# Kernel optimization log

Hardware: AMD Instinct MI355X
Metric: run time of the kernel (lower is better)

Reference implementation:

```python
import jax, jax.numpy as jnp
import numpy as np

B, T, C, H = 4, 1024, 512, 4
D = C // H
N_LAYER, LAYER_ID = 12, 1


def setup_inputs() -> dict:
    key = jax.random.key(0)
    ks = jax.random.split(key, 10)
    w = lambda k, shape: 0.02 * jax.random.normal(k, shape, dtype=jnp.float32)

    r01 = LAYER_ID / (N_LAYER - 1)          # ratio_0_to_1
    r1a0 = 1.0 - LAYER_ID / N_LAYER          # ratio_1_to_almost0
    i = np.arange(C, dtype=np.float32)
    time_decay = (-5.0 + 8.0 * (i / (C - 1)) ** (0.7 + 1.3 * r01)).astype(np.float32)
    xv = i / C
    tm_q = (xv ** r1a0).astype(np.float32)[None, None, :]
    tm_k = (xv ** r1a0).astype(np.float32)[None, None, :]
    tm_v = ((xv ** r1a0) + 0.3 * r01).astype(np.float32)[None, None, :]
    tm_g = (xv ** (0.5 * r1a0)).astype(np.float32)[None, None, :]

    return dict(
        x=jax.random.normal(ks[0], (B, T, C), dtype=jnp.float32),
        ln1_g=jnp.ones((C,), jnp.float32), ln1_b=jnp.zeros((C,), jnp.float32),
        ln2_g=jnp.ones((C,), jnp.float32), ln2_b=jnp.zeros((C,), jnp.float32),
        time_decay=jnp.asarray(time_decay),
        tm_q=jnp.asarray(tm_q), tm_k=jnp.asarray(tm_k),
        tm_v=jnp.asarray(tm_v), tm_g=jnp.asarray(tm_g),
        Wq=w(ks[1], (C, C)), Wk=w(ks[2], (C, C)), Wv=w(ks[3], (C, C)),
        Wg=w(ks[4], (C, C)), Wo=w(ks[5], (C, C)),
        rms_scale=jnp.ones((C,), jnp.float32),
        W1=w(ks[6], (4 * C, C)), W2=w(ks[7], (C, 4 * C)),
    )


def layernorm(x, g, b, eps=1e-5):
    m = x.mean(-1, keepdims=True)
    v = ((x - m) ** 2).mean(-1, keepdims=True)
    return g * (x - m) / jnp.sqrt(v + eps) + b


def rmsnorm(x, scale, eps=1e-8):
    # matches: norm = ||x||_2 / sqrt(dim); out = scale * x / (norm + eps)
    norm = jnp.sqrt(jnp.sum(x * x, axis=-1, keepdims=True)) / (x.shape[-1] ** 0.5)
    return scale * (x / (norm + eps))


def lnssm_scan(q, k, v, lam):
    """Decayed linear-attention scan. q,k,v: [B,T,H,D]; lam: [H,D] (decay over k index).
    Returns S: [B,T,H,D] = q_t^T A_t, Zs: [B,T,H] = q_t . z_t."""
    qT, kT, vT = (jnp.moveaxis(a, 1, 0) for a in (q, k, v))  # [T,B,H,D]
    Bq = q.shape[0]
    A0 = jnp.zeros((Bq, q.shape[2], q.shape[3], q.shape[3]), q.dtype)
    z0 = jnp.zeros((Bq, q.shape[2], q.shape[3]), q.dtype)

    def step(carry, inp):
        A, z = carry
        qt, kt, vt = inp
        A = lam[None, :, :, None] * A + kt[..., None] * vt[..., None, :]  # [B,H,Dk,Dv]
        z = lam[None] * z + kt                                            # [B,H,Dk]
        St = jnp.einsum('bhi,bhij->bhj', qt, A)
        Zt = jnp.einsum('bhi,bhi->bh', qt, z)
        return (A, z), (St, Zt)

    _, (S, Zs) = jax.lax.scan(step, (A0, z0), (qT, kT, vT))
    return jnp.moveaxis(S, 0, 1), jnp.moveaxis(Zs, 0, 1)


def reference(x, ln1_g, ln1_b, ln2_g, ln2_b, time_decay, tm_q, tm_k, tm_v, tm_g,
              Wq, Wk, Wv, Wg, Wo, rms_scale, W1, W2):
    Bx, Tx, Cx = x.shape
    Hh, Dd = H, Cx // H

    # --- TimeMix on ln1(x) ---
    h = layernorm(x, ln1_g, ln1_b)
    xx = jnp.concatenate([jnp.zeros_like(h[:, :1]), h[:, :-1]], axis=1)  # time shift
    xq = h * tm_q + xx * (1 - tm_q)
    xk = h * tm_k + xx * (1 - tm_k)
    xv_ = h * tm_v + xx * (1 - tm_v)
    xg = h * tm_g + xx * (1 - tm_g)
    q = xq @ Wq.T
    k = xk @ Wk.T
    v = xv_ @ Wv.T
    g = jax.nn.sigmoid(xg @ Wg.T)
    q = jnp.exp(rmsnorm(q, rms_scale))
    k = jnp.exp(rmsnorm(k, rms_scale))

    lam = jnp.exp(-jnp.exp(time_decay)).reshape(Hh, Dd)
    qh = q.reshape(Bx, Tx, Hh, Dd)
    kh = k.reshape(Bx, Tx, Hh, Dd)
    vh = v.reshape(Bx, Tx, Hh, Dd)
    S, Zs = lnssm_scan(qh, kh, vh, lam)
    att = (S / Zs[..., None]).reshape(Bx, Tx, Cx)
    att = (g * att) @ Wo.T
    x = x + att

    # --- ChannelMix on ln2(x) ---
    h2 = layernorm(x, ln2_g, ln2_b)
    x = x + jax.nn.gelu(h2 @ W1.T, approximate=False) @ W2.T
    return x
```

## Files before the change

### kernel.cpp

```cpp
#include <hip/hip_runtime.h>
#include <math.h>

#define Bb 4
#define Tt 1024
#define Cc 512
#define Hh 4
#define Dd 128
#define Mrows (Bb*Tt)
#define NC 32
#define CL 32
#define AUGSZ (Dd*(Dd+1))
#define AUGSTRIDE (16*AUGSZ)

typedef unsigned short u16;
typedef __attribute__((ext_vector_type(8))) short bf16x8;
typedef __attribute__((ext_vector_type(4))) float f32x4;

__device__ __forceinline__ float readlane_f(float v, int lane) {
  return __uint_as_float(__builtin_amdgcn_readlane(__float_as_uint(v), lane));
}
__device__ __forceinline__ u16 f2bf(float f) {
  unsigned u = __float_as_uint(f);
  unsigned r = (u + 0x7fffu + ((u >> 16) & 1u)) >> 16;
  return (u16)r;
}
__device__ __forceinline__ unsigned pack2(float a, float b) {
  return (unsigned)f2bf(a) | ((unsigned)f2bf(b) << 16);
}

__global__ __launch_bounds__(256) void ln_kernel(const float* __restrict__ x,
    const float* __restrict__ g, const float* __restrict__ bta, float* __restrict__ out)
{
  int row = blockIdx.x, tid = threadIdx.x;
  const float* xr = x + (size_t)row * Cc;
  float v0 = xr[tid], v1 = xr[tid + 256];
  float s = v0 + v1, s2 = v0*v0 + v1*v1;
  #pragma unroll
  for (int off = 32; off > 0; off >>= 1) {
    s  += __shfl_down(s,  off, 64);
    s2 += __shfl_down(s2, off, 64);
  }
  __shared__ float rs[4], rq[4];
  int w = tid >> 6;
  if ((tid & 63) == 0) { rs[w] = s; rq[w] = s2; }
  __syncthreads();
  float S  = rs[0]+rs[1]+rs[2]+rs[3];
  float S2 = rq[0]+rq[1]+rq[2]+rq[3];
  float mean = S * (1.0f/Cc);
  float var  = S2 * (1.0f/Cc) - mean*mean;
  float inv = rsqrtf(var + 1e-5f);
  out[(size_t)row*Cc + tid]       = g[tid]     * (v0-mean)*inv + bta[tid];
  out[(size_t)row*Cc + tid + 256] = g[tid+256] * (v1-mean)*inv + bta[tid+256];
}

__global__ __launch_bounds__(256) void ln2b_kernel(const float* __restrict__ x,
    const float* __restrict__ p0, const float* __restrict__ p1,
    const float* __restrict__ g, const float* __restrict__ bta,
    float* __restrict__ x1, u16* __restrict__ out)
{
  int row = blockIdx.x, tid = threadIdx.x;
  size_t r0 = (size_t)row * Cc + tid, r1 = r0 + 256;
  float v0 = x[r0] + p0[r0] + p1[r0];
  float v1 = x[r1] + p0[r1] + p1[r1];
  x1[r0] = v0; x1[r1] = v1;
  float s = v0 + v1, s2 = v0*v0 + v1*v1;
  #pragma unroll
  for (int off = 32; off > 0; off >>= 1) {
    s  += __shfl_down(s,  off, 64);
    s2 += __shfl_down(s2, off, 64);
  }
  __shared__ float rs[4], rq[4];
  int w = tid >> 6;
  if ((tid & 63) == 0) { rs[w] = s; rq[w] = s2; }
  __syncthreads();
  float S  = rs[0]+rs[1]+rs[2]+rs[3];
  float S2 = rq[0]+rq[1]+rq[2]+rq[3];
  float mean = S * (1.0f/Cc);
  float var  = S2 * (1.0f/Cc) - mean*mean;
  float inv = rsqrtf(var + 1e-5f);
  int c0 = tid, c1 = tid + 256;
  float o0 = g[c0] * (v0-mean)*inv + bta[c0];
  float o1 = g[c1] * (v1-mean)*inv + bta[c1];
  out[((size_t)(c0 >> 3) * Mrows + row) * 8 + (c0 & 7)] = f2bf(o0);
  out[((size_t)(c1 >> 3) * Mrows + row) * 8 + (c1 & 7)] = f2bf(o1);
}

__device__ __forceinline__ void mix_one(const float* tm, int c0,
    float4 ha, float4 hb, float4 xa, float4 xb, u16* dst, size_t i8)
{
  float4 ta = *(const float4*)(tm + c0);
  float4 tb = *(const float4*)(tm + c0 + 4);
  uint4 o;
  o.x = pack2(ha.x*ta.x + xa.x*(1.f-ta.x), ha.y*ta.y + xa.y*(1.f-ta.y));
  o.y = pack2(ha.z*ta.z + xa.z*(1.f-ta.z), ha.w*ta.w + xa.w*(1.f-ta.w));
  o.z = pack2(hb.x*tb.x + xb.x*(1.f-tb.x), hb.y*tb.y + xb.y*(1.f-tb.y));
  o.w = pack2(hb.z*tb.z + xb.z*(1.f-tb.z), hb.w*tb.w + xb.w*(1.f-tb.w));
  *(uint4*)(dst + i8) = o;
}

__global__ __launch_bounds__(256) void mix_kernel(const float* __restrict__ h,
    const float* __restrict__ tmq, const float* __restrict__ tmk,
    const float* __restrict__ tmv, const float* __restrict__ tmg,
    u16* __restrict__ xqb, u16* __restrict__ xkb,
    u16* __restrict__ xvb, u16* __restrict__ xgb)
{
  int i = blockIdx.x * 256 + threadIdx.x;
  int m = i & 4095, c0 = (i >> 12) << 3;
  const float* hp = h + (size_t)m*Cc + c0;
  float4 ha = *(const float4*)hp, hb = *(const float4*)(hp + 4);
  float4 xa = make_float4(0,0,0,0), xb = make_float4(0,0,0,0);
  if (m & 1023) { xa = *(const float4*)(hp - Cc); xb = *(const float4*)(hp - Cc + 4); }
  size_t i8 = (size_t)i * 8;
  mix_one(tmq, c0, ha, hb, xa, xb, xqb, i8);
  mix_one(tmk, c0, ha, hb, xa, xb, xkb, i8);
  mix_one(tmv, c0, ha, hb, xa, xb, xvb, i8);
  mix_one(tmg, c0, ha, hb, xa, xb, xgb, i8);
}

__global__ __launch_bounds__(256) void wconv_kernel(const float* __restrict__ src,
    u16* __restrict__ out, int K, int nshift)
{
  int i = blockIdx.x * 256 + threadIdx.x;
  int n = i & ((1 << nshift) - 1), kg = i >> nshift;
  const float* p = src + (size_t)n * K + kg * 8;
  float4 a = *(const float4*)p, b = *(const float4*)(p + 4);
  uint4 o;
  o.x = pack2(a.x, a.y); o.y = pack2(a.z, a.w);
  o.z = pack2(b.x, b.y); o.w = pack2(b.z, b.w);
  *(uint4*)(out + (size_t)i * 8) = o;
}

__global__ __launch_bounds__(256) void wconv5_kernel(const float* __restrict__ s0,
    const float* __restrict__ s1, const float* __restrict__ s2,
    const float* __restrict__ s3, const float* __restrict__ s4,
    u16* __restrict__ out)
{
  int wsel = blockIdx.x >> 7;
  const float* src = wsel == 0 ? s0 : wsel == 1 ? s1 : wsel == 2 ? s2 : wsel == 3 ? s3 : s4;
  int i = (blockIdx.x & 127) * 256 + threadIdx.x;
  int n = i & 511, kg = i >> 9;
  const float* p = src + (size_t)n * 512 + kg * 8;
  float4 a = *(const float4*)p, b = *(const float4*)(p + 4);
  uint4 o;
  o.x = pack2(a.x, a.y); o.y = pack2(a.z, a.w);
  o.z = pack2(b.x, b.y); o.w = pack2(b.z, b.w);
  *(uint4*)(out + (size_t)wsel * 262144 + (size_t)i * 8) = o;
}

template<int MR, int NR, int KR>
__device__ __forceinline__ void gemm_core(const u16* __restrict__ A,
    const u16* __restrict__ W, const float* __restrict__ res,
    float* __restrict__ outf, u16* __restrict__ outb, int act,
    int m0, int n0, u16* Asm, u16* Bsm)
{
  const int tid = threadIdx.x, w = tid >> 6, l = tid & 63;
  const int wr = w >> 1, wc = w & 1;
  f32x4 acc[4][4];
  #pragma unroll
  for (int i = 0; i < 4; ++i)
    #pragma unroll
    for (int j = 0; j < 4; ++j) acc[i][j] = (f32x4){0.f,0.f,0.f,0.f};
  const int kgl = l >> 4, rl = l & 15;
  const int q = w * 4;

  #define STAGE(KT, BUF) do {                                               \
    _Pragma("unroll")                                                       \
    for (int ii = 0; ii < 4; ++ii) {                                        \
      int qq = q + ii;                                                      \
      int isB = qq >> 3, idx = qq & 7, kg = idx >> 1, hf = idx & 1;         \
      const u16* src = isB                                                  \
        ? W + ((size_t)((KT)*4 + kg) * NR + n0 + hf*64 + l) * 8             \
        : A + ((size_t)((KT)*4 + kg) * MR + m0 + hf*64 + l) * 8;            \
      u16* dst = (isB ? Bsm : Asm) + (BUF)*4096 + (kg * 128 + hf * 64) * 8; \
      __builtin_amdgcn_global_load_lds(                                     \
          (const __attribute__((address_space(1))) void*)src,               \
          (__attribute__((address_space(3))) void*)dst, 16, 0, 0);          \
    }                                                                       \
  } while (0)

  constexpr int nk = KR >> 5;
  STAGE(0, 0); STAGE(1, 1); STAGE(2, 2);
  for (int kt = 0; kt < nk; ++kt) {
    const int cur = kt & 3;
    if (kt < nk - 2)       asm volatile("s_waitcnt vmcnt(8)" ::: "memory");
    else if (kt == nk - 2) asm volatile("s_waitcnt vmcnt(4)" ::: "memory");
    else                   asm volatile("s_waitcnt vmcnt(0)" ::: "memory");
    __builtin_amdgcn_s_barrier();
    bf16x8 af[4], bfr[4];
    #pragma unroll
    for (int f = 0; f < 4; ++f)
      af[f] = *(const bf16x8*)&Asm[cur*4096 + (kgl*128 + wr*64 + f*16 + rl) * 8];
    #pragma unroll
    for (int f = 0; f < 4; ++f)
      bfr[f] = *(const bf16x8*)&Bsm[cur*4096 + (kgl*128 + wc*64 + f*16 + rl) * 8];
    if (kt + 3 < nk) STAGE(kt + 3, (kt + 3) & 3);
    __builtin_amdgcn_s_setprio(1);
    #pragma unroll
    for (int i = 0; i < 4; ++i)
      #pragma unroll
      for (int j = 0; j < 4; ++j)
        acc[i][j] = __builtin_amdgcn_mfma_f32_16x16x32_bf16(af[i], bfr[j], acc[i][j], 0, 0, 0);
    __builtin_amdgcn_s_setprio(0);
  }
  #undef STAGE

  const int rbase = (l >> 4) * 4, cn = l & 15;
  #pragma unroll
  for (int i = 0; i < 4; ++i) {
    #pragma unroll
    for (int j = 0; j < 4; ++j) {
      #pragma unroll
      for (int r = 0; r < 4; ++r) {
        int m = m0 + wr*64 + i*16 + rbase + r;
        int n = n0 + wc*64 + j*16 + cn;
        float vv = acc[i][j][r];
        if (res) vv += res[(size_t)m * NR + n];
        if (act == 1) vv = 0.5f*vv*(1.f + erff(vv * 0.70710678118f));
        else if (act == 2) vv = 1.f/(1.f + expf(-vv));
        if (outb) outb[((size_t)(n >> 3) * MR + m) * 8 + (n & 7)] = f2bf(vv);
        else outf[(size_t)m * NR + n] = vv;
      }
    }
  }
}

__global__ __launch_bounds__(256) void gemm_qkvg(const u16* __restrict__ xall,
    const u16* __restrict__ Wall, float* __restrict__ outall)
{
  __shared__ __align__(16) u16 Asm[4*4096];
  __shared__ __align__(16) u16 Bsm[4*4096];
  int z = blockIdx.z;
  const size_t E = (size_t)Mrows * Cc;
  gemm_core<Mrows,512,512>(xall + z*E, Wall + (size_t)z*262144, nullptr,
            outall + z*E, nullptr, z == 3 ? 2 : 0,
            blockIdx.y * 128, blockIdx.x * 128, Asm, Bsm);
}

__global__ __launch_bounds__(256) void gemm_wo(const u16* __restrict__ A,
    const u16* __restrict__ W, float* __restrict__ pbuf)
{
  __shared__ __align__(16) u16 Asm[4*4096];
  __shared__ __align__(16) u16 Bsm[4*4096];
  int z = blockIdx.z;
  const size_t E = (size_t)Mrows * Cc;
  gemm_core<Mrows,512,256>(A + (size_t)z*32*Mrows*8, W + (size_t)z*32*512*8, nullptr,
            pbuf + z*E, nullptr, 0, blockIdx.y * 128, blockIdx.x * 128, Asm, Bsm);
}

__global__ __launch_bounds__(256) void gemm_w1(const u16* __restrict__ A,
    const u16* __restrict__ W, u16* __restrict__ outb)
{
  __shared__ __align__(16) u16 Asm[4*4096];
  __shared__ __align__(16) u16 Bsm[4*4096];
  gemm_core<Mrows,2048,512>(A, W, nullptr, nullptr, outb, 1,
            blockIdx.y * 128, blockIdx.x * 128, Asm, Bsm);
}

__global__ __launch_bounds__(256) void gemm_w2(const u16* __restrict__ A,
    const u16* __restrict__ W, float* __restrict__ pbuf)
{
  __shared__ __align__(16) u16 Asm[4*4096];
  __shared__ __align__(16) u16 Bsm[4*4096];
  int z = blockIdx.z;
  const size_t E = (size_t)Mrows * Cc;
  gemm_core<Mrows,512,512>(A + (size_t)z*64*Mrows*8, W + (size_t)z*64*512*8, nullptr,
            pbuf + z*E, nullptr, 0, blockIdx.y * 128, blockIdx.x * 128, Asm, Bsm);
}

__global__ __launch_bounds__(256) void reduce4_kernel(const float* __restrict__ x1,
    const float* __restrict__ p, float* __restrict__ out)
{
  const size_t E = (size_t)Mrows * Cc;
  size_t f = ((size_t)blockIdx.x * 256 + threadIdx.x) * 4;
  float4 a = *(const float4*)(x1 + f);
  float4 q0 = *(const float4*)(p + f);
  float4 q1 = *(const float4*)(p + E + f);
  float4 q2 = *(const float4*)(p + 2*E + f);
  float4 q3 = *(const float4*)(p + 3*E + f);
  float4 o;
  o.x = a.x + q0.x + q1.x + q2.x + q3.x;
  o.y = a.y + q0.y + q1.y + q2.y + q3.y;
  o.z = a.z + q0.z + q1.z + q2.z + q3.z;
  o.w = a.w + q0.w + q1.w + q2.w + q3.w;
  *(float4*)(out + f) = o;
}

__global__ __launch_bounds__(256) void rmsexp_kernel(float* __restrict__ qm,
    float* __restrict__ km, const float* __restrict__ scale)
{
  int row = blockIdx.x, tid = threadIdx.x;
  float* xr = (blockIdx.y ? km : qm) + (size_t)row * Cc;
  float v0 = xr[tid], v1 = xr[tid+256];
  float s2 = v0*v0 + v1*v1;
  #pragma unroll
  for (int off = 32; off > 0; off >>= 1) s2 += __shfl_down(s2, off, 64);
  __shared__ float rq[4];
  int w = tid >> 6;
  if ((tid & 63) == 0) rq[w] = s2;
  __syncthreads();
  float S2 = rq[0]+rq[1]+rq[2]+rq[3];
  float norm = sqrtf(S2) * 0.044194173824159216f;
  float r = 1.f / (norm + 1e-8f);
  xr[tid]     = expf(scale[tid]     * v0 * r);
  xr[tid+256] = expf(scale[tid+256] * v1 * r);
}

__global__ __launch_bounds__(256) void chunk_state_kernel(const float* __restrict__ k,
    const float* __restrict__ v, const float* __restrict__ td, float* __restrict__ Aug)
{
  __shared__ float k_lds[CL][Dd];
  __shared__ float v_lds[CL][Dd];
  int blk = blockIdx.x; int c = blk & (NC-1); int bh = blk >> 5;
  int b = bh >> 2, h = bh & 3;
  int tid = threadIdx.x;
  size_t base = ((size_t)b*Tt + (size_t)c*CL)*Cc + h*Dd;
  #pragma unroll
  for (int r = 0; r < 4; ++r) {
    int idx4 = r*256 + tid;
    int s = idx4 >> 5; int i4 = (idx4 & 31) << 2;
    *(float4*)&k_lds[s][i4] = *(const float4*)&k[base + (size_t)s*Cc + i4];
    *(float4*)&v_lds[s][i4] = *(const float4*)&v[base + (size_t)s*Cc + i4];
  }
  __syncthreads();
  int iq = tid >> 3; int i0 = iq << 2;
  int jg = tid & 7;  int j0 = jg << 4;
  float lam4[4], powv[4], zacc[4];
  #pragma unroll
  for (int ci=0; ci<4; ++ci) {
    lam4[ci] = expf(-expf(td[h*Dd + i0 + ci]));
    powv[ci] = 1.f; zacc[ci] = 0.f;
  }
  float acc[4][16];
  #pragma unroll
  for (int ci=0; ci<4; ++ci)
    #pragma unroll
    for (int jj=0; jj<16; ++jj) acc[ci][jj] = 0.f;

  for (int s = CL-1; s >= 0; --s) {
    float4 k4 = *(const float4*)&k_lds[s][i0];
    float kw0 = powv[0]*k4.x, kw1 = powv[1]*k4.y, kw2 = powv[2]*k4.z, kw3 = powv[3]*k4.w;
    zacc[0]+=kw0; zacc[1]+=kw1; zacc[2]+=kw2; zacc[3]+=kw3;
    #pragma unroll
    for (int q4 = 0; q4 < 4; ++q4) {
      float4 v4 = *(const float4*)&v_lds[s][j0 + q4*4];
      float vv[4] = {v4.x, v4.y, v4.z, v4.w};
      #pragma unroll
      for (int u=0; u<4; ++u) {
        acc[0][q4*4+u] += kw0*vv[u];
        acc[1][q4*4+u] += kw1*vv[u];
        acc[2][q4*4+u] += kw2*vv[u];
        acc[3][q4*4+u] += kw3*vv[u];
      }
    }
    powv[0]*=lam4[0]; powv[1]*=lam4[1]; powv[2]*=lam4[2]; powv[3]*=lam4[3];
  }
  float* aug = Aug + ((size_t)c*16 + bh)*AUGSZ;
  #pragma unroll
  for (int jj=0; jj<16; ++jj) {
    int j = j0 + jj;
    float4 wv = make_float4(acc[0][jj], acc[1][jj], acc[2][jj], acc[3][jj]);
    *(float4*)&aug[(size_t)j*Dd + i0] = wv;
  }
  if (jg == 0)
    *(float4*)&aug[(size_t)Dd*Dd + i0] = make_float4(zacc[0],zacc[1],zacc[2],zacc[3]);
}

__global__ __launch_bounds__(256) void combine_kernel(float* __restrict__ Aug,
    const float* __restrict__ td)
{
  int idx = blockIdx.x*256 + threadIdx.x;
  if (idx >= AUGSZ) return;
  int bh = blockIdx.y; int h = bh & 3;
  int i = idx & (Dd-1);
  float lamL = expf(-expf(td[h*Dd + i]) * (float)CL);
  float* p = Aug + (size_t)bh*AUGSZ + idx;
  float prev = 0.f;
  for (int c = 0; c < NC; ++c) {
    float val = p[(size_t)c*AUGSTRIDE];
    p[(size_t)c*AUGSTRIDE] = prev;
    prev = lamL*prev + val;
  }
}

__global__ __launch_bounds__(256, 2) void scan_out_kernel(const float* __restrict__ q,
    const float* __restrict__ k, const float* __restrict__ v,
    const float* __restrict__ td, const float* __restrict__ Aug,
    const float* __restrict__ gmat, u16* __restrict__ out)
{
  __shared__ float part[4*16*128];
  __shared__ float zpart[4*16];
  int blk = blockIdx.x; int c = blk & (NC-1); int bh = blk >> 5;
  int b = bh >> 2, h = bh & 3;
  int tid = threadIdx.x; int w = tid >> 6, l = tid & 63;
  const size_t base = ((size_t)b*Tt)*Cc + h*Dd;
  const float* augc = Aug + ((size_t)c*16 + bh)*AUGSZ;
  int iq = w*32 + (l & 31);
  float lamv = expf(-expf(td[h*Dd + iq]));
  float lam_s[32];
  #pragma unroll
  for (int ii = 0; ii < 32; ++ii) lam_s[ii] = readlane_f(lamv, ii);

  float A0[32], A1[32];
  {
    const float4* p0 = (const float4*)(augc + (size_t)l*Dd + w*32);
    const float4* p1 = (const float4*)(augc + (size_t)(l+64)*Dd + w*32);
    #pragma unroll
    for (int r = 0; r < 8; ++r) {
      float4 a = p0[r];
      A0[4*r+0]=a.x; A0[4*r+1]=a.y; A0[4*r+2]=a.z; A0[4*r+3]=a.w;
      float4 bb = p1[r];
      A1[4*r+0]=bb.x; A1[4*r+1]=bb.y; A1[4*r+2]=bb.z; A1[4*r+3]=bb.w;
    }
  }
  float z = 0.f;
  if (l < 32) z = augc[(size_t)Dd*Dd + w*32 + l];

  int t0 = c*CL;
  const float* qk_ptr = (l < 32) ? q : k;
  size_t pbase = base + (size_t)t0*Cc;
  float qk = qk_ptr[pbase + iq];
  float v0 = v[pbase + l];
  float v1 = v[pbase + l + 64];

  #pragma unroll
  for (int half = 0; half < 2; ++half) {
    for (int tl = 0; tl < 16; ++tl) {
      int t = half*16 + tl;
      float qk_c = qk, v0c = v0, v1c = v1;
      if (t + 1 < CL) {
        size_t nb = pbase + (size_t)(t+1)*Cc;
        qk = qk_ptr[nb + iq];
        v0 = v[nb + l];
        v1 = v[nb + l + 64];
      }
      float s0 = 0.f, s1 = 0.f;
      #pragma unroll
      for (int ii = 0; ii < 32; ++ii) {
        float qs = readlane_f(qk_c, ii);
        float ks = readlane_f(qk_c, 32 + ii);
        A0[ii] = lam_s[ii]*A0[ii] + ks*v0c;
        A1[ii] = lam_s[ii]*A1[ii] + ks*v1c;
        s0 += qs * A0[ii];
        s1 += qs * A1[ii];
      }
      part[(w*16 + tl)*128 + l]      = s0;
      part[(w*16 + tl)*128 + l + 64] = s1;
      float kme = __shfl(qk_c, (l & 31) + 32);
      float p = 0.f;
      if (l < 32) { z = lamv*z + kme; p = qk_c * z; }
      #pragma unroll
      for (int off = 16; off > 0; off >>= 1) p += __shfl_down(p, off);
      if (l == 0) zpart[w*16 + tl] = p;
    }
    __syncthreads();
    #pragma unroll
    for (int r = 0; r < 8; ++r) {
      int lin = r*256 + tid; int tt = lin >> 7; int j = lin & 127;
      float sv = part[tt*128 + j] + part[(16+tt)*128 + j]
               + part[(32+tt)*128 + j] + part[(48+tt)*128 + j];
      float zv = zpart[tt] + zpart[16+tt] + zpart[32+tt] + zpart[48+tt];
      int m = b*Tt + t0 + half*16 + tt;
      int cc = h*Dd + j;
      float gv = gmat[(size_t)m*Cc + cc];
      out[((size_t)(cc >> 3) * Mrows + m) * 8 + (cc & 7)] = f2bf(gv * sv / zv);
    }
    __syncthreads();
  }
}

extern "C" void kernel_launch(void* const* d_in, const int* in_sizes, int n_in,
                              void* d_out, int out_size, void* d_ws, size_t ws_size,
                              hipStream_t stream) {
  const float* x    = (const float*)d_in[0];
  const float* ln1g = (const float*)d_in[1];
  const float* ln1b = (const float*)d_in[2];
  const float* ln2g = (const float*)d_in[3];
  const float* ln2b = (const float*)d_in[4];
  const float* td   = (const float*)d_in[5];
  const float* tmq  = (const float*)d_in[6];
  const float* tmk  = (const float*)d_in[7];
  const float* tmv  = (const float*)d_in[8];
  const float* tmg  = (const float*)d_in[9];
  const float* Wq   = (const float*)d_in[10];
  const float* Wk   = (const float*)d_in[11];
  const float* Wv   = (const float*)d_in[12];
  const float* Wg   = (const float*)d_in[13];
  const float* Wo   = (const float*)d_in[14];
  const float* rsc  = (const float*)d_in[15];
  const float* W1   = (const float*)d_in[16];
  const float* W2   = (const float*)d_in[17];
  float* ws = (float*)d_ws;
  const size_t E = (size_t)Mrows*Cc;
  float* s0 = ws;
  float* s1 = ws + E;
  float* s2 = ws + 2*E;
  float* s3 = ws + 3*E;
  float* x1 = ws + 4*E;
  u16* xqb = (u16*)(ws + 5*E);
  u16* xkb = xqb + E;
  u16* xvb = xkb + E;
  u16* xgb = xvb + E;
  float* Aug = ws + 7*E;
  u16* midb = (u16*)Aug;
  float* wreg = ws + 7*E + (size_t)NC*16*AUGSZ;
  u16* Wqb = (u16*)wreg;
  u16* W1b = Wqb + 5*262144;
  u16* W2b = W1b + 1048576;
  u16* Wob = Wqb + 4*262144;
  u16* gattb = xqb;
  u16* h2b   = xkb;

  wconv5_kernel<<<640,256,0,stream>>>(Wq, Wk, Wv, Wg, Wo, Wqb);
  wconv_kernel<<<512,256,0,stream>>>(W1, W1b, 512, 11);
  wconv_kernel<<<512,256,0,stream>>>(W2, W2b, 2048, 9);

  ln_kernel<<<Mrows,256,0,stream>>>(x, ln1g, ln1b, s0);
  mix_kernel<<<1024,256,0,stream>>>(s0, tmq,tmk,tmv,tmg, xqb,xkb,xvb,xgb);
  gemm_qkvg<<<dim3(4,32,4),256,0,stream>>>(xqb, Wqb, s0);
  rmsexp_kernel<<<dim3(Mrows,2),256,0,stream>>>(s0, s1, rsc);
  chunk_state_kernel<<<16*NC,256,0,stream>>>(s1, s2, td, Aug);
  combine_kernel<<<dim3((AUGSZ+255)/256,16),256,0,stream>>>(Aug, td);
  scan_out_kernel<<<16*NC,256,0,stream>>>(s0, s1, s2, td, Aug, s3, gattb);
  gemm_wo<<<dim3(4,32,2),256,0,stream>>>(gattb, Wob, s2);
  ln2b_kernel<<<Mrows,256,0,stream>>>(x, s2, s3, ln2g, ln2b, x1, h2b);
  gemm_w1<<<dim3(16,32),256,0,stream>>>(h2b, W1b, midb);
  gemm_w2<<<dim3(4,32,4),256,0,stream>>>(midb, W2b, s0);
  reduce4_kernel<<<2048,256,0,stream>>>(x1, s0, (float*)d_out);
}
```

Measured before the change: 191.5 us.

## Replace sequential per-chunk scan with MFMA chunked linear-attention output

Result: faster. 173.8 us (-9.3%).

```diff
diff --git a/kernel.cpp b/kernel.cpp
--- a/kernel.cpp
+++ b/kernel.cpp
@@ -11,6 +11,7 @@
 #define CL 32
 #define AUGSZ (Dd*(Dd+1))
 #define AUGSTRIDE (16*AUGSZ)
+#define AUGB_CB 18432
 
 typedef unsigned short u16;
 typedef __attribute__((ext_vector_type(8))) short bf16x8;
@@ -365,106 +366,195 @@
     *(float4*)&aug[(size_t)Dd*Dd + i0] = make_float4(zacc[0],zacc[1],zacc[2],zacc[3]);
 }
 
-__global__ __launch_bounds__(256) void combine_kernel(float* __restrict__ Aug,
-    const float* __restrict__ td)
+__global__ __launch_bounds__(256) void combine_kernel(const float* __restrict__ Aug,
+    const float* __restrict__ td, u16* __restrict__ Augb)
 {
   int idx = blockIdx.x*256 + threadIdx.x;
-  if (idx >= AUGSZ) return;
   int bh = blockIdx.y; int h = bh & 3;
-  int i = idx & (Dd-1);
+  int j = idx >> 7, i = idx & 127;
+  size_t aoff = (size_t)(i >> 3) * 1152 + (size_t)j * 8 + (i & 7);
+  if (j >= 129) {
+    for (int c = 0; c < NC; ++c)
+      Augb[((size_t)c*16 + bh)*AUGB_CB + aoff] = 0;
+    return;
+  }
   float lamL = expf(-expf(td[h*Dd + i]) * (float)CL);
-  float* p = Aug + (size_t)bh*AUGSZ + idx;
+  const float* p = Aug + (size_t)bh*AUGSZ + (size_t)j*Dd + i;
   float prev = 0.f;
   for (int c = 0; c < NC; ++c) {
     float val = p[(size_t)c*AUGSTRIDE];
-    p[(size_t)c*AUGSTRIDE] = prev;
+    Augb[((size_t)c*16 + bh)*AUGB_CB + aoff] = f2bf(prev);
     prev = lamL*prev + val;
   }
 }
 
-__global__ __launch_bounds__(256, 2) void scan_out_kernel(const float* __restrict__ q,
-    const float* __restrict__ k, const float* __restrict__ v,
-    const float* __restrict__ td, const float* __restrict__ Aug,
-    const float* __restrict__ gmat, u16* __restrict__ out)
-{
-  __shared__ float part[4*16*128];
-  __shared__ float zpart[4*16];
-  int blk = blockIdx.x; int c = blk & (NC-1); int bh = blk >> 5;
-  int b = bh >> 2, h = bh & 3;
-  int tid = threadIdx.x; int w = tid >> 6, l = tid & 63;
-  const size_t base = ((size_t)b*Tt)*Cc + h*Dd;
-  const float* augc = Aug + ((size_t)c*16 + bh)*AUGSZ;
-  int iq = w*32 + (l & 31);
-  float lamv = expf(-expf(td[h*Dd + iq]));
-  float lam_s[32];
-  #pragma unroll
-  for (int ii = 0; ii < 32; ++ii) lam_s[ii] = readlane_f(lamv, ii);
-
-  float A0[32], A1[32];
+__global__ __launch_bounds__(256, 2) void scan_mfma_kernel(
+    const float* __restrict__ q, const float* __restrict__ k,
+    const float* __restrict__ v, const float* __restrict__ td,
+    const u16* __restrict__ Augb, const float* __restrict__ gmat,
+    u16* __restrict__ out)
+{
+  __shared__ float k_lds[32*192];
+  __shared__ u16  qfrag[32*128];
+  __shared__ u16  vfrag[4*1152];
+  __shared__ float P32[32*33];
+  __shared__ u16  pfrag[32*32];
+  __shared__ float lam_lds[128];
+  __shared__ float zbuf[32];
+
+  const int tid = threadIdx.x;
+  const int blk = blockIdx.x; const int c = blk & 31, bh = blk >> 5;
+  const int b = bh >> 2, h = bh & 3;
+  const int w = tid >> 6, l = tid & 63;
+  const int t = (w << 3) + (l >> 3);
+  const int is = l & 7;
+
+  if (tid < 128) lam_lds[tid] = expf(-expf(td[h*Dd + tid]));
+
+  const size_t rowbase = ((size_t)(b*Tt + c*CL + t))*Cc + h*Dd + is*16;
+
+  float qv[16];
   {
-    const float4* p0 = (const float4*)(augc + (size_t)l*Dd + w*32);
-    const float4* p1 = (const float4*)(augc + (size_t)(l+64)*Dd + w*32);
-    #pragma unroll
-    for (int r = 0; r < 8; ++r) {
-      float4 a = p0[r];
-      A0[4*r+0]=a.x; A0[4*r+1]=a.y; A0[4*r+2]=a.z; A0[4*r+3]=a.w;
-      float4 bb = p1[r];
-      A1[4*r+0]=bb.x; A1[4*r+1]=bb.y; A1[4*r+2]=bb.z; A1[4*r+3]=bb.w;
-    }
-  }
-  float z = 0.f;
-  if (l < 32) z = augc[(size_t)Dd*Dd + w*32 + l];
-
-  int t0 = c*CL;
-  const float* qk_ptr = (l < 32) ? q : k;
-  size_t pbase = base + (size_t)t0*Cc;
-  float qk = qk_ptr[pbase + iq];
-  float v0 = v[pbase + l];
-  float v1 = v[pbase + l + 64];
-
-  #pragma unroll
-  for (int half = 0; half < 2; ++half) {
-    for (int tl = 0; tl < 16; ++tl) {
-      int t = half*16 + tl;
-      float qk_c = qk, v0c = v0, v1c = v1;
-      if (t + 1 < CL) {
-        size_t nb = pbase + (size_t)(t+1)*Cc;
-        qk = qk_ptr[nb + iq];
-        v0 = v[nb + l];
-        v1 = v[nb + l + 64];
+    #pragma unroll
+    for (int c4 = 0; c4 < 4; ++c4) {
+      float4 q4 = *(const float4*)(q + rowbase + c4*4);
+      qv[c4*4+0]=q4.x; qv[c4*4+1]=q4.y; qv[c4*4+2]=q4.z; qv[c4*4+3]=q4.w;
+    }
+    float lt = (float)(t + 1);
+    u16 qt[16];
+    #pragma unroll
+    for (int e = 0; e < 16; ++e) {
+      float el2 = -expf(td[h*Dd + is*16 + e]) * 1.4426950408889634f;
+      qt[e] = f2bf(qv[e] * exp2f(el2 * lt));
+    }
+    #pragma unroll
+    for (int hf = 0; hf < 2; ++hf) {
+      int k8 = is*2 + hf;
+      uint4 pk;
+      pk.x = (unsigned)qt[hf*8+0] | ((unsigned)qt[hf*8+1]<<16);
+      pk.y = (unsigned)qt[hf*8+2] | ((unsigned)qt[hf*8+3]<<16);
+      pk.z = (unsigned)qt[hf*8+4] | ((unsigned)qt[hf*8+5]<<16);
+      pk.w = (unsigned)qt[hf*8+6] | ((unsigned)qt[hf*8+7]<<16);
+      *(uint4*)&qfrag[t*128 + ((k8 ^ (t&7))<<3)] = pk;
+    }
+  }
+  #pragma unroll
+  for (int c4 = 0; c4 < 4; ++c4)
+    *(float4*)&k_lds[t*192 + is*24 + c4*4] = *(const float4*)(k + rowbase + c4*4);
+  #pragma unroll
+  for (int c4 = 0; c4 < 4; ++c4) {
+    float4 v4 = *(const float4*)(v + rowbase + c4*4);
+    int j0 = is*16 + c4*4;
+    vfrag[(t>>3)*1152 + (j0+0)*8 + (t&7)] = f2bf(v4.x);
+    vfrag[(t>>3)*1152 + (j0+1)*8 + (t&7)] = f2bf(v4.y);
+    vfrag[(t>>3)*1152 + (j0+2)*8 + (t&7)] = f2bf(v4.z);
+    vfrag[(t>>3)*1152 + (j0+3)*8 + (t&7)] = f2bf(v4.w);
+  }
+  if (tid < 32) vfrag[(tid>>3)*1152 + 128*8 + (tid&7)] = 0x3F80;
+  if (tid < 240) {
+    #pragma unroll
+    for (int u = 0; u < 2; ++u) {
+      int e = tid*2 + u;
+      int ig = e / 120, rem = e % 120;
+      vfrag[ig*1152 + (129 + rem/8)*8 + (rem&7)] = 0;
+    }
+  }
+  __syncthreads();
+
+  {
+    float lamr[16], wrun[16];
+    #pragma unroll
+    for (int e4 = 0; e4 < 4; ++e4) {
+      float4 l4 = *(const float4*)&lam_lds[is*16 + e4*4];
+      lamr[e4*4+0]=l4.x; lamr[e4*4+1]=l4.y; lamr[e4*4+2]=l4.z; lamr[e4*4+3]=l4.w;
+    }
+    #pragma unroll
+    for (int e = 0; e < 16; ++e) wrun[e] = 1.f;
+    const int smax = (w << 3) + 7;
+    for (int s = smax; s >= 0; --s) {
+      float dot = 0.f;
+      #pragma unroll
+      for (int c4 = 0; c4 < 4; ++c4) {
+        float4 k4 = *(const float4*)&k_lds[s*192 + is*24 + c4*4];
+        dot = fmaf(qv[c4*4+0], k4.x*wrun[c4*4+0], dot);
+        dot = fmaf(qv[c4*4+1], k4.y*wrun[c4*4+1], dot);
+        dot = fmaf(qv[c4*4+2], k4.z*wrun[c4*4+2], dot);
+        dot = fmaf(qv[c4*4+3], k4.w*wrun[c4*4+3], dot);
       }
-      float s0 = 0.f, s1 = 0.f;
+      dot += __shfl_xor(dot, 1);
+      dot += __shfl_xor(dot, 2);
+      dot += __shfl_xor(dot, 4);
+      bool act = (s <= t);
+      if (act && is == 0) P32[t*33 + s] = dot;
+      if (act) {
+        #pragma unroll
+        for (int e = 0; e < 16; ++e) wrun[e] *= lamr[e];
+      }
+    }
+  }
+  __syncthreads();
+  {
+    int tt = tid >> 3, s0 = (tid & 7) * 4;
+    #pragma unroll
+    for (int ss = 0; ss < 4; ++ss) {
+      int s = s0 + ss;
+      float val = (s <= tt) ? P32[tt*33 + s] : 0.f;
+      pfrag[tt*32 + (((s>>3) ^ (tt&3))<<3) + (s&7)] = f2bf(val);
+    }
+  }
+  __syncthreads();
+
+  const int tau = w >> 1;
+  const int jt0 = (w & 1) ? 5 : 0;
+  const int njt = (w & 1) ? 4 : 5;
+  const int rl = l & 15, kg = l >> 4;
+  const int trow = tau*16 + rl;
+  const u16* augb_base = Augb + ((size_t)c*16 + bh)*AUGB_CB;
+
+  bf16x8 aq[4];
+  #pragma unroll
+  for (int kk = 0; kk < 4; ++kk)
+    aq[kk] = *(const bf16x8*)&qfrag[trow*128 + ((((kk<<2)+kg) ^ (trow&7))<<3)];
+  bf16x8 ap = *(const bf16x8*)&pfrag[trow*32 + ((kg ^ (trow&3))<<3)];
+
+  f32x4 acc[5];
+  #pragma unroll
+  for (int u = 0; u < 5; ++u) acc[u] = (f32x4){0.f,0.f,0.f,0.f};
+
+  #pragma unroll
+  for (int u = 0; u < 5; ++u) {
+    if (u < njt) {
+      int jt = jt0 + u;
       #pragma unroll
-      for (int ii = 0; ii < 32; ++ii) {
-        float qs = readlane_f(qk_c, ii);
-        float ks = readlane_f(qk_c, 32 + ii);
-        A0[ii] = lam_s[ii]*A0[ii] + ks*v0c;
-        A1[ii] = lam_s[ii]*A1[ii] + ks*v1c;
-        s0 += qs * A0[ii];
-        s1 += qs * A1[ii];
+      for (int kk = 0; kk < 4; ++kk) {
+        bf16x8 bfr = *(const bf16x8*)&augb_base[(size_t)(((kk<<2)+kg)*1152 + (jt*16 + rl)*8)];
+        acc[u] = __builtin_amdgcn_mfma_f32_16x16x32_bf16(aq[kk], bfr, acc[u], 0, 0, 0);
       }
-      part[(w*16 + tl)*128 + l]      = s0;
-      part[(w*16 + tl)*128 + l + 64] = s1;
-      float kme = __shfl(qk_c, (l & 31) + 32);
-      float p = 0.f;
-      if (l < 32) { z = lamv*z + kme; p = qk_c * z; }
+      bf16x8 bv = *(const bf16x8*)&vfrag[kg*1152 + (jt*16 + rl)*8];
+      acc[u] = __builtin_amdgcn_mfma_f32_16x16x32_bf16(ap, bv, acc[u], 0, 0, 0);
+    }
+  }
+  if ((w & 1) && rl == 0) {
+    #pragma unroll
+    for (int r = 0; r < 4; ++r) zbuf[tau*16 + kg*4 + r] = acc[3][r];
+  }
+  __syncthreads();
+
+  const int nout = (w & 1) ? 3 : 5;
+  #pragma unroll
+  for (int u = 0; u < 5; ++u) {
+    if (u < nout) {
+      int jt = jt0 + u;
+      int cc = h*Dd + jt*16 + rl;
       #pragma unroll
-      for (int off = 16; off > 0; off >>= 1) p += __shfl_down(p, off);
-      if (l == 0) zpart[w*16 + tl] = p;
-    }
-    __syncthreads();
-    #pragma unroll
-    for (int r = 0; r < 8; ++r) {
-      int lin = r*256 + tid; int tt = lin >> 7; int j = lin & 127;
-      float sv = part[tt*128 + j] + part[(16+tt)*128 + j]
-               + part[(32+tt)*128 + j] + part[(48+tt)*128 + j];
-      float zv = zpart[tt] + zpart[16+tt] + zpart[32+tt] + zpart[48+tt];
-      int m = b*Tt + t0 + half*16 + tt;
-      int cc = h*Dd + j;
-      float gv = gmat[(size_t)m*Cc + cc];
-      out[((size_t)(cc >> 3) * Mrows + m) * 8 + (cc & 7)] = f2bf(gv * sv / zv);
-    }
-    __syncthreads();
+      for (int r = 0; r < 4; ++r) {
+        int tr = tau*16 + kg*4 + r;
+        int m = b*Tt + c*CL + tr;
+        float zv = zbuf[tr];
+        float gv = gmat[(size_t)m*Cc + cc];
+        out[((size_t)(cc >> 3) * Mrows + m) * 8 + (cc & 7)] = f2bf(gv * acc[u][r] / zv);
+      }
+    }
   }
 }
 
@@ -507,6 +597,7 @@
   u16* W1b = Wqb + 5*262144;
   u16* W2b = W1b + 1048576;
   u16* Wob = Wqb + 4*262144;
+  u16* Augb = W2b + 1048576;
   u16* gattb = xqb;
   u16* h2b   = xkb;
 
@@ -519,8 +610,8 @@
   gemm_qkvg<<<dim3(4,32,4),256,0,stream>>>(xqb, Wqb, s0);
   rmsexp_kernel<<<dim3(Mrows,2),256,0,stream>>>(s0, s1, rsc);
   chunk_state_kernel<<<16*NC,256,0,stream>>>(s1, s2, td, Aug);
-  combine_kernel<<<dim3((AUGSZ+255)/256,16),256,0,stream>>>(Aug, td);
-  scan_out_kernel<<<16*NC,256,0,stream>>>(s0, s1, s2, td, Aug, s3, gattb);
+  combine_kernel<<<dim3(72,16),256,0,stream>>>(Aug, td, Augb);
+  scan_mfma_kernel<<<16*NC,256,0,stream>>>(s0, s1, s2, td, Augb, s3, gattb);
   gemm_wo<<<dim3(4,32,2),256,0,stream>>>(gattb, Wob, s2);
   ln2b_kernel<<<Mrows,256,0,stream>>>(x, s2, s3, ln2g, ln2b, x1, h2b);
   gemm_w1<<<dim3(16,32),256,0,stream>>>(h2b, W1b, midb);
```
